# Kernel optimization log

Measured on AMD Instinct MI355X. Metric: run time of the kernel, lower is better.

The kernel has to match this reference:

```python
import jax, jax.numpy as jnp
import numpy as np

B, N, K = 4, 8192, 32
C_IN, C_MID, C_OUT = 64, 64, 128


def _uniform(key, shape, fan_in):
    s = 1.0 / np.sqrt(fan_in).astype(np.float32)
    return jax.random.uniform(key, shape, minval=-s, maxval=s, dtype=jnp.float32)


def setup_inputs() -> dict:
    key = jax.random.key(0)
    ks = jax.random.split(key, 8)
    p = jax.random.normal(ks[0], (B, N, 3), dtype=jnp.float32)
    f = jax.random.normal(ks[1], (B, C_IN, N), dtype=jnp.float32)
    dp = jax.random.normal(ks[2], (B, 3, N, K), dtype=jnp.float32)
    fj = jax.random.normal(ks[3], (B, C_IN, N, K), dtype=jnp.float32)
    # Conv2d 1x1 weights (PyTorch default kaiming-uniform-ish fan-in init)
    W1 = _uniform(ks[4], (C_MID, C_IN + 3), C_IN + 3)
    b1 = _uniform(ks[5], (C_MID,), C_IN + 3)
    W2 = _uniform(ks[6], (C_OUT, C_MID), C_MID)
    b2 = _uniform(ks[7], (C_OUT,), C_MID)
    return {"p": p, "f": f, "dp": dp, "fj": fj, "W1": W1, "b1": b1, "W2": W2, "b2": b2}


def reference(p, f, dp, fj, W1, b1, W2, b2):
    # fj <- cat([dp, fj], dim=1): [B, 3+C_in, N, K]
    x = jnp.concatenate([dp, fj], axis=1)
    # 1x1 Conv2d + ReLU (norm is None in source), layer 1: [B, C_mid, N, K]
    h = jax.nn.relu(jnp.einsum('oc,bcnk->bonk', W1, x) + b1[None, :, None, None])
    # layer 2 (use_res=False, is_head=False -> ReLU on last layer too): [B, C_out, N, K]
    h = jax.nn.relu(jnp.einsum('oc,bcnk->bonk', W2, h) + b2[None, :, None, None])
    # max-pool over neighbor axis K: [B, C_out, N]
    return jnp.max(h, axis=-1)
```

## Files before the change

kernel.cpp:

```cpp
#include <hip/hip_runtime.h>
#include <hip/hip_bf16.h>
#include <stdint.h>

#define B_    4
#define N_    8192
#define K_    32
#define CX    67
#define CMID  64
#define COUT  128

#define CSTR  100
#define HSTR  72
#define TPG   8
#define NWG   1024
#define GMAX  8191

typedef __bf16 bf16_t;
typedef bf16_t bf16x8 __attribute__((ext_vector_type(8)));
typedef bf16_t bf16x4 __attribute__((ext_vector_type(4)));
typedef float  f32x4  __attribute__((ext_vector_type(4)));

__device__ __forceinline__ uint32_t pack2bf(float a, float b) {
    union { bf16_t h[2]; uint32_t u; } x;
    x.h[0] = (bf16_t)a; x.h[1] = (bf16_t)b;
    return x.u;
}

template<bool DIRECT>
__global__ __launch_bounds__(256, 2)
void sa_main(const float* __restrict__ dp, const float* __restrict__ fj,
             const float* __restrict__ W1, const float* __restrict__ b1,
             const float* __restrict__ W2, const float* __restrict__ b2,
             float* __restrict__ dst)
{
    __shared__ bf16_t smem[4 * 32 * CSTR + 4 * 16 * HSTR];

    const int tid  = threadIdx.x;
    const int wave = tid >> 6;
    const int lane = tid & 63;
    const int lrow = lane & 15;
    const int g    = lane >> 4;

    bf16_t* Xw = smem + wave * 32 * CSTR;
    bf16_t* Hw = smem + 4 * 32 * CSTR + wave * 16 * HSTR;

    const size_t plane = (size_t)N_ * K_;
    const int cr = lane >> 3;
    const int k0 = (lane & 7) << 2;

    auto issue = [&](float4 (&v)[9], int Gi) {
        const int bb = Gi >> 11;
        const int nn = ((Gi & 2047) << 2) + wave;
        const size_t rbase = (size_t)nn * K_ + k0;
        const float* fp  = fj + (size_t)bb * 64 * plane + rbase;
        const float* dp0 = dp + (size_t)bb * 3  * plane + rbase;
        const float* p0 = (cr < 3) ? dp0 + (size_t)cr * plane
                                   : fp  + (size_t)(cr - 3) * plane;
        v[0] = *(const float4*)p0;
        const float* pj = fp + (size_t)(8 + cr - 3) * plane;
        #pragma unroll
        for (int j = 1; j < 8; ++j) {
            v[j] = *(const float4*)pj;
            pj += 8 * plane;
        }
        const int c8 = (cr < 3) ? (64 + cr) : 66;
        v[8] = *(const float4*)(fp + (size_t)(c8 - 3) * plane);
    };

    float4 va[9], vb[9];
    {
        const int G0 = blockIdx.x * TPG;
        issue(va, G0);
        issue(vb, G0 + 1 > GMAX ? GMAX : G0 + 1);
    }

    for (int i = tid; i < 64 * 96; i += 256) {
        int o = i / 96, c = i - o * 96;
        smem[i] = (c < CX) ? (bf16_t)W1[o * CX + c] : (bf16_t)0.f;
    }
    __syncthreads();
    bf16x8 w1f[3][4];
    #pragma unroll
    for (int kc = 0; kc < 3; ++kc)
        #pragma unroll
        for (int rt = 0; rt < 4; ++rt)
            w1f[kc][rt] = *(const bf16x8*)&smem[(rt * 16 + lrow) * 96 + kc * 32 + g * 8];
    __syncthreads();
    for (int i = tid; i < 128 * 72; i += 256) {
        int o = i / 72, c = i - o * 72;
        smem[i] = (c < CMID) ? (bf16_t)W2[o * CMID + c] : (bf16_t)0.f;
    }
    __syncthreads();
    bf16x8 w2f[2][8];
    #pragma unroll
    for (int kc = 0; kc < 2; ++kc)
        #pragma unroll
        for (int ot = 0; ot < 8; ++ot)
            w2f[kc][ot] = *(const bf16x8*)&smem[(ot * 16 + lrow) * 72 + kc * 32 + g * 8];
    __syncthreads();
    for (int i = tid; i < 4 * 32 * CSTR; i += 256) smem[i] = (bf16_t)0.f;
    __syncthreads();

    f32x4 b1f[4];
    #pragma unroll
    for (int rt = 0; rt < 4; ++rt) b1f[rt] = *(const f32x4*)(b1 + rt * 16 + g * 4);
    float b2f[8];
    #pragma unroll
    for (int ot = 0; ot < 8; ++ot) b2f[ot] = b2[ot * 16 + lrow];

    auto point = [&](float4 (&v)[9], int G) {
        const int b = G >> 11;
        const int n = ((G & 2047) << 2) + wave;

        #pragma unroll
        for (int j = 0; j < 9; ++j) {
            int c = j * 8 + cr;
            if (c < CX) {
                Xw[(k0 + 0) * CSTR + c] = (bf16_t)v[j].x;
                Xw[(k0 + 1) * CSTR + c] = (bf16_t)v[j].y;
                Xw[(k0 + 2) * CSTR + c] = (bf16_t)v[j].z;
                Xw[(k0 + 3) * CSTR + c] = (bf16_t)v[j].w;
            }
        }
        {
            int Gn = G + 2;
            if (Gn > GMAX) Gn = GMAX;
            issue(v, Gn);
        }

        float macc[8];
        #pragma unroll
        for (int i = 0; i < 8; ++i) macc[i] = -3e38f;

        #pragma unroll
        for (int ct = 0; ct < 2; ++ct) {
            const int col = ct * 16 + lrow;
            f32x4 acc1[4] = {};
            __builtin_amdgcn_s_setprio(1);
            #pragma unroll
            for (int kc = 0; kc < 3; ++kc) {
                bf16x4 lo = *(const bf16x4*)&Xw[col * CSTR + kc * 32 + g * 8];
                bf16x4 hi = *(const bf16x4*)&Xw[col * CSTR + kc * 32 + g * 8 + 4];
                bf16x8 bfX = __builtin_shufflevector(lo, hi, 0, 1, 2, 3, 4, 5, 6, 7);
                #pragma unroll
                for (int rt = 0; rt < 4; ++rt)
                    acc1[rt] = __builtin_amdgcn_mfma_f32_16x16x32_bf16(w1f[kc][rt], bfX, acc1[rt], 0, 0, 0);
            }
            __builtin_amdgcn_s_setprio(0);
            #pragma unroll
            for (int rt = 0; rt < 4; ++rt) {
                float h0 = fmaxf(acc1[rt][0] + b1f[rt][0], 0.f);
                float h1 = fmaxf(acc1[rt][1] + b1f[rt][1], 0.f);
                float h2 = fmaxf(acc1[rt][2] + b1f[rt][2], 0.f);
                float h3 = fmaxf(acc1[rt][3] + b1f[rt][3], 0.f);
                *(uint2*)&Hw[lrow * HSTR + rt * 16 + g * 4] =
                    make_uint2(pack2bf(h0, h1), pack2bf(h2, h3));
            }
            bf16x8 hb0 = *(const bf16x8*)&Hw[lrow * HSTR +  0 + g * 8];
            bf16x8 hb1 = *(const bf16x8*)&Hw[lrow * HSTR + 32 + g * 8];
            __builtin_amdgcn_s_setprio(1);
            #pragma unroll
            for (int bt = 0; bt < 2; ++bt) {
                f32x4 a2[4] = {};
                #pragma unroll
                for (int o = 0; o < 4; ++o) {
                    a2[o] = __builtin_amdgcn_mfma_f32_16x16x32_bf16(hb0, w2f[0][bt * 4 + o], a2[o], 0, 0, 0);
                    a2[o] = __builtin_amdgcn_mfma_f32_16x16x32_bf16(hb1, w2f[1][bt * 4 + o], a2[o], 0, 0, 0);
                }
                #pragma unroll
                for (int o = 0; o < 4; ++o) {
                    float m = fmaxf(fmaxf(a2[o][0], a2[o][1]), fmaxf(a2[o][2], a2[o][3]));
                    macc[bt * 4 + o] = fmaxf(macc[bt * 4 + o], m);
                }
            }
            __builtin_amdgcn_s_setprio(0);
        }

        #pragma unroll
        for (int ot = 0; ot < 8; ++ot) {
            float vv = macc[ot];
            vv = fmaxf(vv, __shfl_xor(vv, 16, 64));
            vv = fmaxf(vv, __shfl_xor(vv, 32, 64));
            macc[ot] = fmaxf(vv + b2f[ot], 0.f);
        }
        float oa = (g == 0) ? macc[0] : (g == 1) ? macc[2] : (g == 2) ? macc[4] : macc[6];
        float ob = (g == 0) ? macc[1] : (g == 1) ? macc[3] : (g == 2) ? macc[5] : macc[7];
        const int ca = g * 32 + lrow;
        const int cb = g * 32 + 16 + lrow;
        if (DIRECT) {
            float* op = dst + (size_t)b * COUT * N_ + n;
            op[(size_t)ca * N_] = oa;
            op[(size_t)cb * N_] = ob;
        } else {
            float* wp = dst + ((size_t)(b * N_ + n)) * COUT;
            wp[ca] = oa;
            wp[cb] = ob;
        }
    };

    #pragma unroll 1
    for (int t = 0; t < TPG; t += 2) {
        const int G = blockIdx.x * TPG + t;
        point(va, G);
        point(vb, G + 1);
    }
}

__global__ __launch_bounds__(256)
void sa_transpose(const float* __restrict__ ws, float* __restrict__ out)
{
    __shared__ float tile[32][136];
    const int t  = threadIdx.x;
    const int i  = blockIdx.x;
    const int b  = i >> 8;
    const int n0 = (i & 255) << 5;

    const float* rp = ws + ((size_t)(b * N_ + n0)) * COUT;
    #pragma unroll
    for (int r = 0; r < 4; ++r) {
        int flat = (r * 256 + t) * 4;
        int nl = flat >> 7, c = flat & 127;
        float4 v = *(const float4*)(rp + (size_t)nl * COUT + c);
        *(float4*)&tile[nl][c] = v;
    }
    __syncthreads();
    float* op = out + (size_t)b * COUT * N_ + n0;
    const int nl4 = (t & 7) << 2;
    #pragma unroll
    for (int r2 = 0; r2 < 4; ++r2) {
        int c = r2 * 32 + (t >> 3);
        float4 o4;
        o4.x = tile[nl4 + 0][c];
        o4.y = tile[nl4 + 1][c];
        o4.z = tile[nl4 + 2][c];
        o4.w = tile[nl4 + 3][c];
        *(float4*)(op + (size_t)c * N_ + nl4) = o4;
    }
}

extern "C" void kernel_launch(void* const* d_in, const int* in_sizes, int n_in,
                              void* d_out, int out_size, void* d_ws, size_t ws_size,
                              hipStream_t stream) {
    const float* dp = (const float*)d_in[2];
    const float* fj = (const float*)d_in[3];
    const float* W1 = (const float*)d_in[4];
    const float* b1 = (const float*)d_in[5];
    const float* W2 = (const float*)d_in[6];
    const float* b2 = (const float*)d_in[7];
    float* out = (float*)d_out;

    const size_t ws_need = (size_t)B_ * N_ * COUT * sizeof(float);
    if (ws_size >= ws_need) {
        float* ws = (float*)d_ws;
        hipLaunchKernelGGL((sa_main<false>), dim3(NWG), dim3(256), 0, stream,
                           dp, fj, W1, b1, W2, b2, ws);
        hipLaunchKernelGGL(sa_transpose, dim3(1024), dim3(256), 0, stream, ws, out);
    } else {
        hipLaunchKernelGGL((sa_main<true>), dim3(NWG), dim3(256), 0, stream,
                           dp, fj, W1, b1, W2, b2, out);
    }
}
```

Measured before the change: 115.0 us.

## Load inputs directly into MFMA fragments, keep weights in LDS, raise occupancy

Each lane now loads scalar floats laid out to match the MFMA B-fragment (16 neighbors × 8 channels) and packs them to bf16 in registers. This removes the LDS transpose staging buffer for X and its scattered scalar stores. Weights for both layers stay in LDS and are re-read per MFMA instead of being held in registers. That frees registers so launch bounds can go to 3 blocks per CU, with TPG halved and twice as many workgroups. The cost is scalar (non-vectorized) global loads and extra LDS reads of the weights on every tile.

```diff
diff --git a/kernel.cpp b/kernel.cpp
--- a/kernel.cpp
+++ b/kernel.cpp
@@ -9,15 +9,18 @@
 #define CMID  64
 #define COUT  128
 
-#define CSTR  100
-#define HSTR  72
-#define TPG   8
-#define NWG   1024
+#define W1S   104
+#define W2S   72
+#define TPG   4
+#define NWG   2048
 #define GMAX  8191
+
+#define W1E   (64 * W1S)
+#define HB0   (W1E + 128 * W2S)
+#define SMEME (HB0 + 4 * 32 * W2S)
 
 typedef __bf16 bf16_t;
 typedef bf16_t bf16x8 __attribute__((ext_vector_type(8)));
-typedef bf16_t bf16x4 __attribute__((ext_vector_type(4)));
 typedef float  f32x4  __attribute__((ext_vector_type(4)));
 
 __device__ __forceinline__ uint32_t pack2bf(float a, float b) {
@@ -27,13 +30,13 @@
 }
 
 template<bool DIRECT>
-__global__ __launch_bounds__(256, 2)
+__global__ __launch_bounds__(256, 3)
 void sa_main(const float* __restrict__ dp, const float* __restrict__ fj,
              const float* __restrict__ W1, const float* __restrict__ b1,
              const float* __restrict__ W2, const float* __restrict__ b2,
              float* __restrict__ dst)
 {
-    __shared__ bf16_t smem[4 * 32 * CSTR + 4 * 16 * HSTR];
+    __shared__ bf16_t smem[SMEME];
 
     const int tid  = threadIdx.x;
     const int wave = tid >> 6;
@@ -41,64 +44,51 @@
     const int lrow = lane & 15;
     const int g    = lane >> 4;
 
-    bf16_t* Xw = smem + wave * 32 * CSTR;
-    bf16_t* Hw = smem + 4 * 32 * CSTR + wave * 16 * HSTR;
-
     const size_t plane = (size_t)N_ * K_;
-    const int cr = lane >> 3;
-    const int k0 = (lane & 7) << 2;
-
-    auto issue = [&](float4 (&v)[9], int Gi) {
-        const int bb = Gi >> 11;
-        const int nn = ((Gi & 2047) << 2) + wave;
-        const size_t rbase = (size_t)nn * K_ + k0;
-        const float* fp  = fj + (size_t)bb * 64 * plane + rbase;
-        const float* dp0 = dp + (size_t)bb * 3  * plane + rbase;
-        const float* p0 = (cr < 3) ? dp0 + (size_t)cr * plane
-                                   : fp  + (size_t)(cr - 3) * plane;
-        v[0] = *(const float4*)p0;
-        const float* pj = fp + (size_t)(8 + cr - 3) * plane;
-        #pragma unroll
-        for (int j = 1; j < 8; ++j) {
-            v[j] = *(const float4*)pj;
-            pj += 8 * plane;
-        }
-        const int c8 = (cr < 3) ? (64 + cr) : 66;
-        v[8] = *(const float4*)(fp + (size_t)(c8 - 3) * plane);
+    const int bidx = blockIdx.x;
+    const int b    = (bidx * TPG) >> 11;
+
+    const float* dpb = dp + (size_t)b * 3  * plane;
+    const float* fjb = fj + (size_t)b * 64 * plane;
+
+    const float* baseA = (g == 0) ? dpb
+                       : fjb + (ptrdiff_t)(8 * g - 3) * (ptrdiff_t)plane;
+    const float* baseB = fjb + (ptrdiff_t)(8 * g - 3) * (ptrdiff_t)plane;
+    const float* base1 = fjb + (size_t)(29 + 8 * g) * plane;
+    const float* base2 = fjb + (size_t)61 * plane;
+
+    float la[19], lb[19];
+    auto issue = [&](int G) {
+        const int n = ((G & 2047) << 2) + wave;
+        const size_t off = (size_t)n * K_ + lrow;
+        const float* pA = baseA + off;
+        const float* pB = baseB + off;
+        const float* p1 = base1 + off;
+        #pragma unroll
+        for (int e = 0; e < 3; ++e) { la[e]   = pA[(size_t)e * plane]; lb[e]   = pA[(size_t)e * plane + 16]; }
+        #pragma unroll
+        for (int e = 3; e < 8; ++e) { la[e]   = pB[(size_t)e * plane]; lb[e]   = pB[(size_t)e * plane + 16]; }
+        #pragma unroll
+        for (int e = 0; e < 8; ++e) { la[8+e] = p1[(size_t)e * plane]; lb[8+e] = p1[(size_t)e * plane + 16]; }
+        la[16] = la[17] = la[18] = 0.f;
+        lb[16] = lb[17] = lb[18] = 0.f;
+        if (g == 0) {
+            const float* p2 = base2 + off;
+            #pragma unroll
+            for (int e = 0; e < 3; ++e) { la[16+e] = p2[(size_t)e * plane]; lb[16+e] = p2[(size_t)e * plane + 16]; }
+        }
     };
 
-    float4 va[9], vb[9];
-    {
-        const int G0 = blockIdx.x * TPG;
-        issue(va, G0);
-        issue(vb, G0 + 1 > GMAX ? GMAX : G0 + 1);
-    }
-
-    for (int i = tid; i < 64 * 96; i += 256) {
-        int o = i / 96, c = i - o * 96;
+    issue(bidx * TPG);
+
+    for (int i = tid; i < W1E; i += 256) {
+        int o = i / W1S, c = i - o * W1S;
         smem[i] = (c < CX) ? (bf16_t)W1[o * CX + c] : (bf16_t)0.f;
     }
-    __syncthreads();
-    bf16x8 w1f[3][4];
-    #pragma unroll
-    for (int kc = 0; kc < 3; ++kc)
-        #pragma unroll
-        for (int rt = 0; rt < 4; ++rt)
-            w1f[kc][rt] = *(const bf16x8*)&smem[(rt * 16 + lrow) * 96 + kc * 32 + g * 8];
-    __syncthreads();
-    for (int i = tid; i < 128 * 72; i += 256) {
-        int o = i / 72, c = i - o * 72;
-        smem[i] = (c < CMID) ? (bf16_t)W2[o * CMID + c] : (bf16_t)0.f;
-    }
-    __syncthreads();
-    bf16x8 w2f[2][8];
-    #pragma unroll
-    for (int kc = 0; kc < 2; ++kc)
-        #pragma unroll
-        for (int ot = 0; ot < 8; ++ot)
-            w2f[kc][ot] = *(const bf16x8*)&smem[(ot * 16 + lrow) * 72 + kc * 32 + g * 8];
-    __syncthreads();
-    for (int i = tid; i < 4 * 32 * CSTR; i += 256) smem[i] = (bf16_t)0.f;
+    for (int i = tid; i < 128 * W2S; i += 256) {
+        int o = i / W2S, c = i - o * W2S;
+        smem[W1E + i] = (c < CMID) ? (bf16_t)W2[o * CMID + c] : (bf16_t)0.f;
+    }
     __syncthreads();
 
     f32x4 b1f[4];
@@ -108,73 +98,93 @@
     #pragma unroll
     for (int ot = 0; ot < 8; ++ot) b2f[ot] = b2[ot * 16 + lrow];
 
-    auto point = [&](float4 (&v)[9], int G) {
-        const int b = G >> 11;
+    bf16_t* Hw = smem + HB0 + wave * 32 * W2S;
+    const bf16_t* W2l = smem + W1E;
+
+    #pragma unroll 1
+    for (int t = 0; t < TPG; ++t) {
+        const int G = bidx * TPG + t;
         const int n = ((G & 2047) << 2) + wave;
 
-        #pragma unroll
-        for (int j = 0; j < 9; ++j) {
-            int c = j * 8 + cr;
-            if (c < CX) {
-                Xw[(k0 + 0) * CSTR + c] = (bf16_t)v[j].x;
-                Xw[(k0 + 1) * CSTR + c] = (bf16_t)v[j].y;
-                Xw[(k0 + 2) * CSTR + c] = (bf16_t)v[j].z;
-                Xw[(k0 + 3) * CSTR + c] = (bf16_t)v[j].w;
+        bf16x8 f0[3], f1[3];
+        {
+            union { uint32_t u[4]; bf16x8 v; } cv;
+            cv.u[0] = pack2bf(la[0], la[1]);   cv.u[1] = pack2bf(la[2], la[3]);
+            cv.u[2] = pack2bf(la[4], la[5]);   cv.u[3] = pack2bf(la[6], la[7]);   f0[0] = cv.v;
+            cv.u[0] = pack2bf(la[8], la[9]);   cv.u[1] = pack2bf(la[10], la[11]);
+            cv.u[2] = pack2bf(la[12], la[13]); cv.u[3] = pack2bf(la[14], la[15]); f0[1] = cv.v;
+            cv.u[0] = pack2bf(la[16], la[17]); cv.u[1] = pack2bf(la[18], 0.f);
+            cv.u[2] = 0;                       cv.u[3] = 0;                       f0[2] = cv.v;
+            cv.u[0] = pack2bf(lb[0], lb[1]);   cv.u[1] = pack2bf(lb[2], lb[3]);
+            cv.u[2] = pack2bf(lb[4], lb[5]);   cv.u[3] = pack2bf(lb[6], lb[7]);   f1[0] = cv.v;
+            cv.u[0] = pack2bf(lb[8], lb[9]);   cv.u[1] = pack2bf(lb[10], lb[11]);
+            cv.u[2] = pack2bf(lb[12], lb[13]); cv.u[3] = pack2bf(lb[14], lb[15]); f1[1] = cv.v;
+            cv.u[0] = pack2bf(lb[16], lb[17]); cv.u[1] = pack2bf(lb[18], 0.f);
+            cv.u[2] = 0;                       cv.u[3] = 0;                       f1[2] = cv.v;
+        }
+        { int Gn = G + 1; if (Gn > GMAX) Gn = GMAX; issue(Gn); }
+
+        f32x4 acc0[4] = {}, acc1v[4] = {};
+        __builtin_amdgcn_s_setprio(1);
+        #pragma unroll
+        for (int kc = 0; kc < 3; ++kc) {
+            #pragma unroll
+            for (int rt = 0; rt < 4; ++rt) {
+                bf16x8 wf = *(const bf16x8*)&smem[(rt * 16 + lrow) * W1S + kc * 32 + g * 8];
+                acc0[rt]  = __builtin_amdgcn_mfma_f32_16x16x32_bf16(wf, f0[kc], acc0[rt], 0, 0, 0);
+                acc1v[rt] = __builtin_amdgcn_mfma_f32_16x16x32_bf16(wf, f1[kc], acc1v[rt], 0, 0, 0);
             }
         }
-        {
-            int Gn = G + 2;
-            if (Gn > GMAX) Gn = GMAX;
-            issue(v, Gn);
-        }
+        __builtin_amdgcn_s_setprio(0);
+
+        #pragma unroll
+        for (int rt = 0; rt < 4; ++rt) {
+            float h0 = fmaxf(acc0[rt][0] + b1f[rt][0], 0.f);
+            float h1 = fmaxf(acc0[rt][1] + b1f[rt][1], 0.f);
+            float h2 = fmaxf(acc0[rt][2] + b1f[rt][2], 0.f);
+            float h3 = fmaxf(acc0[rt][3] + b1f[rt][3], 0.f);
+            *(uint2*)&Hw[lrow * W2S + rt * 16 + g * 4] =
+                make_uint2(pack2bf(h0, h1), pack2bf(h2, h3));
+            float j0 = fmaxf(acc1v[rt][0] + b1f[rt][0], 0.f);
+            float j1 = fmaxf(acc1v[rt][1] + b1f[rt][1], 0.f);
+            float j2 = fmaxf(acc1v[rt][2] + b1f[rt][2], 0.f);
+            float j3 = fmaxf(acc1v[rt][3] + b1f[rt][3], 0.f);
+            *(uint2*)&Hw[(16 + lrow) * W2S + rt * 16 + g * 4] =
+                make_uint2(pack2bf(j0, j1), pack2bf(j2, j3));
+        }
+
+        bf16x8 hb00 = *(const bf16x8*)&Hw[lrow * W2S + g * 8];
+        bf16x8 hb01 = *(const bf16x8*)&Hw[lrow * W2S + 32 + g * 8];
+        bf16x8 hb10 = *(const bf16x8*)&Hw[(16 + lrow) * W2S + g * 8];
+        bf16x8 hb11 = *(const bf16x8*)&Hw[(16 + lrow) * W2S + 32 + g * 8];
 
         float macc[8];
-        #pragma unroll
-        for (int i = 0; i < 8; ++i) macc[i] = -3e38f;
-
-        #pragma unroll
-        for (int ct = 0; ct < 2; ++ct) {
-            const int col = ct * 16 + lrow;
-            f32x4 acc1[4] = {};
-            __builtin_amdgcn_s_setprio(1);
-            #pragma unroll
-            for (int kc = 0; kc < 3; ++kc) {
-                bf16x4 lo = *(const bf16x4*)&Xw[col * CSTR + kc * 32 + g * 8];
-                bf16x4 hi = *(const bf16x4*)&Xw[col * CSTR + kc * 32 + g * 8 + 4];
-                bf16x8 bfX = __builtin_shufflevector(lo, hi, 0, 1, 2, 3, 4, 5, 6, 7);
+        __builtin_amdgcn_s_setprio(1);
+        #pragma unroll
+        for (int bt = 0; bt < 2; ++bt) {
+            f32x4 a20[4] = {}, a21[4] = {};
+            #pragma unroll
+            for (int o = 0; o < 4; ++o) {
                 #pragma unroll
-                for (int rt = 0; rt < 4; ++rt)
-                    acc1[rt] = __builtin_amdgcn_mfma_f32_16x16x32_bf16(w1f[kc][rt], bfX, acc1[rt], 0, 0, 0);
-            }
-            __builtin_amdgcn_s_setprio(0);
-            #pragma unroll
-            for (int rt = 0; rt < 4; ++rt) {
-                float h0 = fmaxf(acc1[rt][0] + b1f[rt][0], 0.f);
-                float h1 = fmaxf(acc1[rt][1] + b1f[rt][1], 0.f);
-                float h2 = fmaxf(acc1[rt][2] + b1f[rt][2], 0.f);
-                float h3 = fmaxf(acc1[rt][3] + b1f[rt][3], 0.f);
-                *(uint2*)&Hw[lrow * HSTR + rt * 16 + g * 4] =
-                    make_uint2(pack2bf(h0, h1), pack2bf(h2, h3));
-            }
-            bf16x8 hb0 = *(const bf16x8*)&Hw[lrow * HSTR +  0 + g * 8];
-            bf16x8 hb1 = *(const bf16x8*)&Hw[lrow * HSTR + 32 + g * 8];
-            __builtin_amdgcn_s_setprio(1);
-            #pragma unroll
-            for (int bt = 0; bt < 2; ++bt) {
-                f32x4 a2[4] = {};
-                #pragma unroll
-                for (int o = 0; o < 4; ++o) {
-                    a2[o] = __builtin_amdgcn_mfma_f32_16x16x32_bf16(hb0, w2f[0][bt * 4 + o], a2[o], 0, 0, 0);
-                    a2[o] = __builtin_amdgcn_mfma_f32_16x16x32_bf16(hb1, w2f[1][bt * 4 + o], a2[o], 0, 0, 0);
-                }
-                #pragma unroll
-                for (int o = 0; o < 4; ++o) {
-                    float m = fmaxf(fmaxf(a2[o][0], a2[o][1]), fmaxf(a2[o][2], a2[o][3]));
-                    macc[bt * 4 + o] = fmaxf(macc[bt * 4 + o], m);
+                for (int kc2 = 0; kc2 < 2; ++kc2) {
+                    bf16x8 wf = *(const bf16x8*)&W2l[((bt * 4 + o) * 16 + lrow) * W2S + kc2 * 32 + g * 8];
+                    if (kc2 == 0) {
+                        a20[o] = __builtin_amdgcn_mfma_f32_16x16x32_bf16(hb00, wf, a20[o], 0, 0, 0);
+                        a21[o] = __builtin_amdgcn_mfma_f32_16x16x32_bf16(hb10, wf, a21[o], 0, 0, 0);
+                    } else {
+                        a20[o] = __builtin_amdgcn_mfma_f32_16x16x32_bf16(hb01, wf, a20[o], 0, 0, 0);
+                        a21[o] = __builtin_amdgcn_mfma_f32_16x16x32_bf16(hb11, wf, a21[o], 0, 0, 0);
+                    }
                 }
             }
-            __builtin_amdgcn_s_setprio(0);
-        }
+            #pragma unroll
+            for (int o = 0; o < 4; ++o) {
+                float m0 = fmaxf(fmaxf(a20[o][0], a20[o][1]), fmaxf(a20[o][2], a20[o][3]));
+                float m1 = fmaxf(fmaxf(a21[o][0], a21[o][1]), fmaxf(a21[o][2], a21[o][3]));
+                macc[bt * 4 + o] = fmaxf(m0, m1);
+            }
+        }
+        __builtin_amdgcn_s_setprio(0);
 
         #pragma unroll
         for (int ot = 0; ot < 8; ++ot) {
@@ -196,13 +206,6 @@
             wp[ca] = oa;
             wp[cb] = ob;
         }
-    };
-
-    #pragma unroll 1
-    for (int t = 0; t < TPG; t += 2) {
-        const int G = blockIdx.x * TPG + t;
-        point(va, G);
-        point(vb, G + 1);
     }
 }
 
```

After: 120.7 us. 1.05x slower.

## Keep layer-1 output in registers by permuting W1 rows, dropping H staging in LDS

Applied to the files above, without the earlier changes.

Rows of W1 and b1 are permuted so the layer-1 MFMA accumulator layout lines up with the B-operand layout of the layer-2 MFMA. The hidden activations can then be packed to bf16 in registers rather than written to and reread from a shared-memory H buffer. Layer 2 now takes H as the A operand, and each lane reads two neighbour rows (2*lrow, 2*lrow+1) with single 16-byte LDS loads, using a new padded X stride of 104. Prefetch drops from two points in flight to one, which lowers register pressure but reduces how much global-load latency is hidden.

```diff
diff --git a/kernel.cpp b/kernel.cpp
--- a/kernel.cpp
+++ b/kernel.cpp
@@ -9,15 +9,13 @@
 #define CMID  64
 #define COUT  128
 
-#define CSTR  100
-#define HSTR  72
+#define CSTR  104
 #define TPG   8
 #define NWG   1024
 #define GMAX  8191
 
 typedef __bf16 bf16_t;
 typedef bf16_t bf16x8 __attribute__((ext_vector_type(8)));
-typedef bf16_t bf16x4 __attribute__((ext_vector_type(4)));
 typedef float  f32x4  __attribute__((ext_vector_type(4)));
 
 __device__ __forceinline__ uint32_t pack2bf(float a, float b) {
@@ -33,7 +31,7 @@
              const float* __restrict__ W2, const float* __restrict__ b2,
              float* __restrict__ dst)
 {
-    __shared__ bf16_t smem[4 * 32 * CSTR + 4 * 16 * HSTR];
+    __shared__ bf16_t smem[4 * 32 * CSTR];
 
     const int tid  = threadIdx.x;
     const int wave = tid >> 6;
@@ -42,13 +40,16 @@
     const int g    = lane >> 4;
 
     bf16_t* Xw = smem + wave * 32 * CSTR;
-    bf16_t* Hw = smem + 4 * 32 * CSTR + wave * 16 * HSTR;
 
     const size_t plane = (size_t)N_ * K_;
+    const int bidx = blockIdx.x;
+    const int b    = (bidx * TPG) >> 11;
+
     const int cr = lane >> 3;
     const int k0 = (lane & 7) << 2;
 
-    auto issue = [&](float4 (&v)[9], int Gi) {
+    float4 v[9];
+    auto issue = [&](int Gi) {
         const int bb = Gi >> 11;
         const int nn = ((Gi & 2047) << 2) + wave;
         const size_t rbase = (size_t)nn * K_ + k0;
@@ -67,15 +68,12 @@
         v[8] = *(const float4*)(fp + (size_t)(c8 - 3) * plane);
     };
 
-    float4 va[9], vb[9];
-    {
-        const int G0 = blockIdx.x * TPG;
-        issue(va, G0);
-        issue(vb, G0 + 1 > GMAX ? GMAX : G0 + 1);
-    }
+    issue(bidx * TPG);
 
     for (int i = tid; i < 64 * 96; i += 256) {
-        int o = i / 96, c = i - o * 96;
+        int s = i / 96, c = i - s * 96;
+        int rt = s >> 4, rr = s & 15, qq = rr >> 2, ii = rr & 3;
+        int o = 32 * (rt >> 1) + 8 * qq + 4 * (rt & 1) + ii;
         smem[i] = (c < CX) ? (bf16_t)W1[o * CX + c] : (bf16_t)0.f;
     }
     __syncthreads();
@@ -93,23 +91,25 @@
     __syncthreads();
     bf16x8 w2f[2][8];
     #pragma unroll
-    for (int kc = 0; kc < 2; ++kc)
+    for (int kcc = 0; kcc < 2; ++kcc)
         #pragma unroll
         for (int ot = 0; ot < 8; ++ot)
-            w2f[kc][ot] = *(const bf16x8*)&smem[(ot * 16 + lrow) * 72 + kc * 32 + g * 8];
+            w2f[kcc][ot] = *(const bf16x8*)&smem[(ot * 16 + lrow) * 72 + kcc * 32 + g * 8];
     __syncthreads();
     for (int i = tid; i < 4 * 32 * CSTR; i += 256) smem[i] = (bf16_t)0.f;
     __syncthreads();
 
     f32x4 b1f[4];
     #pragma unroll
-    for (int rt = 0; rt < 4; ++rt) b1f[rt] = *(const f32x4*)(b1 + rt * 16 + g * 4);
+    for (int rt = 0; rt < 4; ++rt)
+        b1f[rt] = *(const f32x4*)(b1 + 32 * (rt >> 1) + 8 * g + 4 * (rt & 1));
     float b2f[8];
     #pragma unroll
     for (int ot = 0; ot < 8; ++ot) b2f[ot] = b2[ot * 16 + lrow];
 
-    auto point = [&](float4 (&v)[9], int G) {
-        const int b = G >> 11;
+    #pragma unroll 1
+    for (int t = 0; t < TPG; ++t) {
+        const int G = bidx * TPG + t;
         const int n = ((G & 2047) << 2) + wave;
 
         #pragma unroll
@@ -122,59 +122,81 @@
                 Xw[(k0 + 3) * CSTR + c] = (bf16_t)v[j].w;
             }
         }
+        { int Gn = G + 1; if (Gn > GMAX) Gn = GMAX; issue(Gn); }
+
+        bf16x8 f0[3], f1[3];
+        #pragma unroll
+        for (int kc = 0; kc < 3; ++kc) {
+            f0[kc] = *(const bf16x8*)&Xw[(2 * lrow)     * CSTR + kc * 32 + g * 8];
+            f1[kc] = *(const bf16x8*)&Xw[(2 * lrow + 1) * CSTR + kc * 32 + g * 8];
+        }
+
+        bf16x8 a2f0[2], a2f1[2];
         {
-            int Gn = G + 2;
-            if (Gn > GMAX) Gn = GMAX;
-            issue(v, Gn);
+            f32x4 acc[4] = {};
+            __builtin_amdgcn_s_setprio(1);
+            #pragma unroll
+            for (int kc = 0; kc < 3; ++kc)
+                #pragma unroll
+                for (int rt = 0; rt < 4; ++rt)
+                    acc[rt] = __builtin_amdgcn_mfma_f32_16x16x32_bf16(w1f[kc][rt], f0[kc], acc[rt], 0, 0, 0);
+            __builtin_amdgcn_s_setprio(0);
+            #pragma unroll
+            for (int kc2 = 0; kc2 < 2; ++kc2) {
+                union { uint32_t u[4]; bf16x8 w; } cc;
+                #pragma unroll
+                for (int hh = 0; hh < 2; ++hh) {
+                    const int rt = 2 * kc2 + hh;
+                    float h0 = fmaxf(acc[rt][0] + b1f[rt][0], 0.f);
+                    float h1 = fmaxf(acc[rt][1] + b1f[rt][1], 0.f);
+                    float h2 = fmaxf(acc[rt][2] + b1f[rt][2], 0.f);
+                    float h3 = fmaxf(acc[rt][3] + b1f[rt][3], 0.f);
+                    cc.u[hh * 2 + 0] = pack2bf(h0, h1);
+                    cc.u[hh * 2 + 1] = pack2bf(h2, h3);
+                }
+                a2f0[kc2] = cc.w;
+            }
+        }
+        {
+            f32x4 acc[4] = {};
+            __builtin_amdgcn_s_setprio(1);
+            #pragma unroll
+            for (int kc = 0; kc < 3; ++kc)
+                #pragma unroll
+                for (int rt = 0; rt < 4; ++rt)
+                    acc[rt] = __builtin_amdgcn_mfma_f32_16x16x32_bf16(w1f[kc][rt], f1[kc], acc[rt], 0, 0, 0);
+            __builtin_amdgcn_s_setprio(0);
+            #pragma unroll
+            for (int kc2 = 0; kc2 < 2; ++kc2) {
+                union { uint32_t u[4]; bf16x8 w; } cc;
+                #pragma unroll
+                for (int hh = 0; hh < 2; ++hh) {
+                    const int rt = 2 * kc2 + hh;
+                    float h0 = fmaxf(acc[rt][0] + b1f[rt][0], 0.f);
+                    float h1 = fmaxf(acc[rt][1] + b1f[rt][1], 0.f);
+                    float h2 = fmaxf(acc[rt][2] + b1f[rt][2], 0.f);
+                    float h3 = fmaxf(acc[rt][3] + b1f[rt][3], 0.f);
+                    cc.u[hh * 2 + 0] = pack2bf(h0, h1);
+                    cc.u[hh * 2 + 1] = pack2bf(h2, h3);
+                }
+                a2f1[kc2] = cc.w;
+            }
         }
 
         float macc[8];
-        #pragma unroll
-        for (int i = 0; i < 8; ++i) macc[i] = -3e38f;
-
-        #pragma unroll
-        for (int ct = 0; ct < 2; ++ct) {
-            const int col = ct * 16 + lrow;
-            f32x4 acc1[4] = {};
-            __builtin_amdgcn_s_setprio(1);
-            #pragma unroll
-            for (int kc = 0; kc < 3; ++kc) {
-                bf16x4 lo = *(const bf16x4*)&Xw[col * CSTR + kc * 32 + g * 8];
-                bf16x4 hi = *(const bf16x4*)&Xw[col * CSTR + kc * 32 + g * 8 + 4];
-                bf16x8 bfX = __builtin_shufflevector(lo, hi, 0, 1, 2, 3, 4, 5, 6, 7);
-                #pragma unroll
-                for (int rt = 0; rt < 4; ++rt)
-                    acc1[rt] = __builtin_amdgcn_mfma_f32_16x16x32_bf16(w1f[kc][rt], bfX, acc1[rt], 0, 0, 0);
-            }
-            __builtin_amdgcn_s_setprio(0);
-            #pragma unroll
-            for (int rt = 0; rt < 4; ++rt) {
-                float h0 = fmaxf(acc1[rt][0] + b1f[rt][0], 0.f);
-                float h1 = fmaxf(acc1[rt][1] + b1f[rt][1], 0.f);
-                float h2 = fmaxf(acc1[rt][2] + b1f[rt][2], 0.f);
-                float h3 = fmaxf(acc1[rt][3] + b1f[rt][3], 0.f);
-                *(uint2*)&Hw[lrow * HSTR + rt * 16 + g * 4] =
-                    make_uint2(pack2bf(h0, h1), pack2bf(h2, h3));
-            }
-            bf16x8 hb0 = *(const bf16x8*)&Hw[lrow * HSTR +  0 + g * 8];
-            bf16x8 hb1 = *(const bf16x8*)&Hw[lrow * HSTR + 32 + g * 8];
-            __builtin_amdgcn_s_setprio(1);
-            #pragma unroll
-            for (int bt = 0; bt < 2; ++bt) {
-                f32x4 a2[4] = {};
-                #pragma unroll
-                for (int o = 0; o < 4; ++o) {
-                    a2[o] = __builtin_amdgcn_mfma_f32_16x16x32_bf16(hb0, w2f[0][bt * 4 + o], a2[o], 0, 0, 0);
-                    a2[o] = __builtin_amdgcn_mfma_f32_16x16x32_bf16(hb1, w2f[1][bt * 4 + o], a2[o], 0, 0, 0);
-                }
-                #pragma unroll
-                for (int o = 0; o < 4; ++o) {
-                    float m = fmaxf(fmaxf(a2[o][0], a2[o][1]), fmaxf(a2[o][2], a2[o][3]));
-                    macc[bt * 4 + o] = fmaxf(macc[bt * 4 + o], m);
-                }
-            }
-            __builtin_amdgcn_s_setprio(0);
-        }
+        __builtin_amdgcn_s_setprio(1);
+        #pragma unroll
+        for (int ot = 0; ot < 8; ++ot) {
+            f32x4 t0 = {}, t1 = {};
+            t0 = __builtin_amdgcn_mfma_f32_16x16x32_bf16(a2f0[0], w2f[0][ot], t0, 0, 0, 0);
+            t0 = __builtin_amdgcn_mfma_f32_16x16x32_bf16(a2f0[1], w2f[1][ot], t0, 0, 0, 0);
+            t1 = __builtin_amdgcn_mfma_f32_16x16x32_bf16(a2f1[0], w2f[0][ot], t1, 0, 0, 0);
+            t1 = __builtin_amdgcn_mfma_f32_16x16x32_bf16(a2f1[1], w2f[1][ot], t1, 0, 0, 0);
+            float m0 = fmaxf(fmaxf(t0[0], t0[1]), fmaxf(t0[2], t0[3]));
+            float m1 = fmaxf(fmaxf(t1[0], t1[1]), fmaxf(t1[2], t1[3]));
+            macc[ot] = fmaxf(m0, m1);
+        }
+        __builtin_amdgcn_s_setprio(0);
 
         #pragma unroll
         for (int ot = 0; ot < 8; ++ot) {
@@ -185,24 +207,17 @@
         }
         float oa = (g == 0) ? macc[0] : (g == 1) ? macc[2] : (g == 2) ? macc[4] : macc[6];
         float ob = (g == 0) ? macc[1] : (g == 1) ? macc[3] : (g == 2) ? macc[5] : macc[7];
-        const int ca = g * 32 + lrow;
-        const int cb = g * 32 + 16 + lrow;
+        const int ca  = g * 32 + lrow;
+        const int cb2 = g * 32 + 16 + lrow;
         if (DIRECT) {
             float* op = dst + (size_t)b * COUT * N_ + n;
-            op[(size_t)ca * N_] = oa;
-            op[(size_t)cb * N_] = ob;
+            op[(size_t)ca  * N_] = oa;
+            op[(size_t)cb2 * N_] = ob;
         } else {
             float* wp = dst + ((size_t)(b * N_ + n)) * COUT;
-            wp[ca] = oa;
-            wp[cb] = ob;
-        }
-    };
-
-    #pragma unroll 1
-    for (int t = 0; t < TPG; t += 2) {
-        const int G = blockIdx.x * TPG + t;
-        point(va, G);
-        point(vb, G + 1);
+            wp[ca]  = oa;
+            wp[cb2] = ob;
+        }
     }
 }
 
```

Measured after the change: 112.5 us. 1.02x faster.
